# Kernel optimization log

Measured on AMD Instinct MI355X. Metric: run time of the kernel, lower is better.

## Reference

```python
import jax, jax.numpy as jnp
import numpy as np
import math

B, N, D, K = 4, 255, 256, 128
NODE_FEATURES_OFFSET = 128
MAX_Z = 101
NUM_EDGES = 2 * NODE_FEATURES_OFFSET + 1  # 257
NUM_DIR_KERNEL = 128  # FourierDirectionalEmbed num_kernel
ECFG_F = 20  # synthetic electron-config feature dim


def setup_inputs() -> dict:
    key = jax.random.key(0)
    ks = jax.random.split(key, 16)
    positions = jax.random.normal(ks[0], (B, N, 3), dtype=jnp.float32) * 3.0
    atomic_numbers = jax.random.randint(ks[1], (B, N), 1, MAX_Z, dtype=jnp.int32)
    s = 0.02
    emb_z = jax.random.normal(ks[2], (MAX_Z + 1, D), dtype=jnp.float32) * s
    electron_config = jax.random.uniform(ks[3], (MAX_Z + 1, ECFG_F), dtype=jnp.float32)
    config_W = jax.random.normal(ks[4], (ECFG_F, D), dtype=jnp.float32) * s
    config_b = jnp.zeros((D,), dtype=jnp.float32)
    mult_W = jax.random.normal(ks[5], (NODE_FEATURES_OFFSET, D), dtype=jnp.float32) * s
    charge_W = jax.random.normal(ks[6], (NODE_FEATURES_OFFSET, D), dtype=jnp.float32) * s
    gbf_means = jax.random.uniform(ks[7], (K,), dtype=jnp.float32, minval=0.0, maxval=7.0)
    gbf_stds = jax.random.uniform(ks[8], (K,), dtype=jnp.float32, minval=0.0, maxval=3.0)
    gbf_mul = jax.random.normal(ks[9], (NUM_EDGES,), dtype=jnp.float32).at[0].set(0.0)  # padding_idx=0
    gbf_bias = (jax.random.normal(ks[10], (NUM_EDGES,), dtype=jnp.float32) * 0.1).at[0].set(0.0)
    proj1_W = jax.random.normal(ks[11], (K, K), dtype=jnp.float32) * (1.0 / math.sqrt(K))
    proj1_b = jnp.zeros((K,), dtype=jnp.float32)
    proj2_W = jax.random.normal(ks[12], (K, D), dtype=jnp.float32) * (1.0 / math.sqrt(K))
    proj2_b = jnp.zeros((D,), dtype=jnp.float32)
    dir_W = jax.random.normal(ks[13], (2 * NUM_DIR_KERNEL, D), dtype=jnp.float32) * (1.0 / math.sqrt(2 * NUM_DIR_KERNEL))
    dir_b = jnp.zeros((D,), dtype=jnp.float32)
    return dict(positions=positions, atomic_numbers=atomic_numbers, emb_z=emb_z,
                electron_config=electron_config, config_W=config_W, config_b=config_b,
                mult_W=mult_W, charge_W=charge_W, gbf_means=gbf_means, gbf_stds=gbf_stds,
                gbf_mul=gbf_mul, gbf_bias=gbf_bias, proj1_W=proj1_W, proj1_b=proj1_b,
                proj2_W=proj2_W, proj2_b=proj2_b, dir_W=dir_W, dir_b=dir_b)


def _angular_freqs():
    min_angle = 1e-4
    half = NUM_DIR_KERNEL // 2
    wl_az = jnp.exp(jnp.linspace(math.log(2 * min_angle), math.log(2 * 2 * math.pi), half))
    wl_po = jnp.exp(jnp.linspace(math.log(2 * min_angle), math.log(2 * math.pi), half))
    return (2 * math.pi / wl_az).astype(jnp.float32), (2 * math.pi / wl_po).astype(jnp.float32)


def _forward(positions, atomic_numbers, emb_z, electron_config, config_W, config_b,
             mult_W, charge_W, gbf_means, gbf_stds, gbf_mul, gbf_bias,
             proj1_W, proj1_b, proj2_W, proj2_b, dir_W, dir_b):
    b = positions.shape[0]
    # add graph-level (CLS) token: zero position, z = MAX_Z = 101
    pos = jnp.concatenate([jnp.zeros_like(positions[:, :1]), positions], axis=1)  # [B,Np,3]
    z = jnp.concatenate([jnp.full_like(atomic_numbers[:, :1], MAX_Z), atomic_numbers], axis=1)  # [B,Np]
    npad = pos.shape[1]

    # --- node embedding: nuclear + electronic + multiplicity(1) + charge(0) ---
    elec = electron_config[z] @ config_W + config_b            # [B,Np,D]
    elec = elec.at[:, 0, :].set(0.0)                            # cls_token row zeroed
    node = emb_z[z] + elec + mult_W[1] + charge_W[0]           # [B,Np,D]

    # --- pairwise geometry: directions[b,i,j] = pos[j] - pos[i] ---
    d = pos[:, None, :, :] - pos[:, :, None, :]                # [B,Np,Np,3]
    sq = jnp.sum(d * d, axis=-1)
    dist = jnp.sqrt(sq + 1e-12)                                # [B,Np,Np]
    nd = d / (dist[..., None] + 1e-5)                          # normed directions, eps per source
    eye = jnp.eye(npad, dtype=bool)[None, :, :]
    x_safe = jnp.where(eye, 1.0, nd[..., 0])
    y_safe = jnp.where(eye, 0.0, nd[..., 1])
    azimuth = jnp.arctan2(y_safe, x_safe)                      # [B,Np,Np]
    polar = jnp.arccos(jnp.clip(nd[..., 2], -1.0 + 1e-6, 1.0 - 1e-6))

    # --- FourierDirectionalEmbed ---
    f_az, f_po = _angular_freqs()
    ph_az = azimuth[..., None] * f_az                          # [B,Np,Np,64]
    ph_po = polar[..., None] * f_po
    sinusoids = jnp.concatenate([jnp.sin(ph_az), jnp.cos(ph_az),
                                 jnp.sin(ph_po), jnp.cos(ph_po)], axis=-1)  # [B,Np,Np,256]
    dir_out = sinusoids @ dir_W + dir_b                        # [B,Np,Np,D]

    # --- Gaussian3DEmbed ---
    zi = z[:, :, None]
    zj = z[:, None, :] + NODE_FEATURES_OFFSET
    mul = gbf_mul[zi] + gbf_mul[zj]                            # sum over the 2 edge-type entries
    bias = gbf_bias[zi] + gbf_bias[zj]                         # [B,Np,Np]
    gx = (mul * dist + bias)[..., None]                        # [B,Np,Np,1] -> broadcast to K
    std = jnp.abs(gbf_stds) + 0.01
    pi_c = 3.14159
    gauss = jnp.exp(-0.5 * ((gx - gbf_means) / std) ** 2) / ((2 * pi_c) ** 0.5 * std)  # [B,Np,Np,K]
    h = jax.nn.gelu(gauss @ proj1_W + proj1_b, approximate=False)
    gbf_out = h @ proj2_W + proj2_b                            # [B,Np,Np,D]

    return node, gbf_out, dir_out


def reference(positions, atomic_numbers, emb_z, electron_config, config_W, config_b,
              mult_W, charge_W, gbf_means, gbf_stds, gbf_mul, gbf_bias,
              proj1_W, proj1_b, proj2_W, proj2_b, dir_W, dir_b):
    return _forward(positions, atomic_numbers, emb_z, electron_config, config_W, config_b,
                    mult_W, charge_W, gbf_means, gbf_stds, gbf_mul, gbf_bias,
                    proj1_W, proj1_b, proj2_W, proj2_b, dir_W, dir_b)
```

## Files before the change

kernel.cpp:

```cpp
#include <hip/hip_runtime.h>
#include <math.h>

typedef __bf16 bf16x8 __attribute__((ext_vector_type(8)));
typedef __bf16 bf16x4 __attribute__((ext_vector_type(4)));
typedef float f32x4 __attribute__((ext_vector_type(4)));

#define PI_D 3.14159265358979323846

__global__ void prep_kernel(const float* __restrict__ dir_W,
                            const float* __restrict__ proj1_W,
                            const float* __restrict__ proj2_W,
                            const float* __restrict__ gbf_stds,
                            __bf16* __restrict__ dirP, __bf16* __restrict__ p1P,
                            __bf16* __restrict__ p2P,
                            float* __restrict__ f_az, float* __restrict__ f_po,
                            float* __restrict__ inv_std, float* __restrict__ coef) {
  int tid = threadIdx.x + blockIdx.x * blockDim.x;
  int nth = gridDim.x * blockDim.x;
  for (int o = tid; o < 256 * 256; o += nth) {
    int j = o & 7, l = (o >> 3) & 63, ks = (o >> 9) & 7, nt = o >> 12;
    int d = nt * 16 + (l & 15);
    int s = ks * 32 + (l >> 4) * 8 + j;
    dirP[o] = (__bf16)dir_W[s * 256 + d];
  }
  for (int o = tid; o < 128 * 128; o += nth) {
    int j = o & 7, l = (o >> 3) & 63, ks = (o >> 9) & 3, nt = o >> 11;
    int ko = nt * 16 + (l & 15);
    int ki = ks * 32 + (l >> 4) * 8 + j;
    p1P[o] = (__bf16)proj1_W[ki * 128 + ko];
  }
  for (int o = tid; o < 128 * 256; o += nth) {
    int j = o & 7, l = (o >> 3) & 63, ks = (o >> 9) & 3, nt = o >> 11;
    int d = nt * 16 + (l & 15);
    int k = ks * 32 + (l >> 4) * 8 + j;
    p2P[o] = (__bf16)proj2_W[k * 256 + d];
  }
  if (blockIdx.x == 0 && threadIdx.x < 64) {
    int q = threadIdx.x;
    double l0 = log(2.0 * 1e-4);
    double l1a = log(2.0 * 2.0 * PI_D);
    double l1p = log(2.0 * PI_D);
    double ta = l0 + (l1a - l0) * (double)q / 63.0;
    double tp = l0 + (l1p - l0) * (double)q / 63.0;
    f_az[q] = (float)(2.0 * PI_D / exp(ta));
    f_po[q] = (float)(2.0 * PI_D / exp(tp));
  }
  if (blockIdx.x == 1 && threadIdx.x < 128) {
    int k = threadIdx.x;
    float sd = fabsf(gbf_stds[k]) + 0.01f;
    inv_std[k] = 1.0f / sd;
    coef[k] = (float)(1.0 / (sqrt(2.0 * 3.14159) * (double)sd));
  }
}

__global__ void node_kernel(const int* __restrict__ an, const float* __restrict__ emb_z,
                            const float* __restrict__ ec, const float* __restrict__ cW,
                            const float* __restrict__ cb, const float* __restrict__ mult_W,
                            const float* __restrict__ charge_W, float* __restrict__ out_node) {
  int bi = blockIdx.x;
  int b = bi >> 8, i = bi & 255;
  int d = threadIdx.x;
  int z = (i == 0) ? 101 : an[b * 255 + i - 1];
  float elec = 0.0f;
  if (i != 0) {
    for (int f = 0; f < 20; ++f) elec += ec[z * 20 + f] * cW[f * 256 + d];
    elec += cb[d];
  }
  float v = emb_z[z * 256 + d] + elec + mult_W[256 + d] + charge_W[d];
  out_node[(size_t)bi * 256 + d] = v;
}

__global__ __launch_bounds__(256, 4) void pair_kernel(
    const float* __restrict__ positions, const int* __restrict__ atomic_numbers,
    const float* __restrict__ gbf_means, const float* __restrict__ gbf_mul,
    const float* __restrict__ gbf_bias, const float* __restrict__ proj1_b,
    const float* __restrict__ proj2_b, const float* __restrict__ dir_b,
    const __bf16* __restrict__ dirP, const __bf16* __restrict__ p1P,
    const __bf16* __restrict__ p2P, const float* __restrict__ f_az,
    const float* __restrict__ f_po, const float* __restrict__ inv_stdv,
    const float* __restrict__ coefv, float* __restrict__ out_gbf,
    float* __restrict__ out_dir) {
  __shared__ __align__(16) __bf16 buf[64 * 136];
  __shared__ float s_az[64], s_po[64], s_gx[64];

  const int tid = threadIdx.x;
  const int bid = blockIdx.x;
  const int jt = bid & 3;
  const int i = (bid >> 2) & 255;
  const int b = bid >> 10;
  const int j0 = jt * 64;
  const long pairbase = ((long)(b * 256 + i)) * 256 + j0;

  const int lane = tid & 63, wv = tid >> 6;
  const int lr = lane & 15, kb = lane >> 4;

  if (tid < 64) {
    int p = tid, j = j0 + p;
    float pxi = 0.f, pyi = 0.f, pzi = 0.f, pxj = 0.f, pyj = 0.f, pzj = 0.f;
    if (i != 0) { const float* q = positions + ((size_t)b * 255 + (i - 1)) * 3; pxi = q[0]; pyi = q[1]; pzi = q[2]; }
    if (j != 0) { const float* q = positions + ((size_t)b * 255 + (j - 1)) * 3; pxj = q[0]; pyj = q[1]; pzj = q[2]; }
    float dx = pxj - pxi, dy = pyj - pyi, dz = pzj - pzi;
    float sq = dx * dx + dy * dy + dz * dz;
    float dist = sqrtf(sq + 1e-12f);
    float inv = 1.0f / (dist + 1e-5f);
    float ndx = dx * inv, ndy = dy * inv, ndz = dz * inv;
    bool diag = (i == j);
    float xs = diag ? 1.0f : ndx;
    float ys = diag ? 0.0f : ndy;
    s_az[p] = atan2f(ys, xs);
    float cz = fminf(fmaxf(ndz, -1.0f + 1e-6f), 1.0f - 1e-6f);
    s_po[p] = acosf(cz);
    int zi = (i == 0) ? 101 : atomic_numbers[b * 255 + i - 1];
    int zj = ((j == 0) ? 101 : atomic_numbers[b * 255 + j - 1]) + 128;
    float mul = gbf_mul[zi] + gbf_mul[zj];
    float bia = gbf_bias[zi] + gbf_bias[zj];
    s_gx[p] = mul * dist + bia;
  }
  __syncthreads();

  f32x4 acc[4][4];
#pragma unroll
  for (int mtl = 0; mtl < 4; ++mtl)
#pragma unroll
    for (int np = 0; np < 4; ++np) acc[mtl][np] = (f32x4){0.f, 0.f, 0.f, 0.f};

  for (int half = 0; half < 2; ++half) {
#pragma unroll
    for (int it = 0; it < 2; ++it) {
      int job = tid + it * 256;
      int p = job >> 3, g = job & 7;
      int q0 = g * 8;
      float ang = half ? s_po[p] : s_az[p];
      const float* ft = half ? f_po : f_az;
      bf16x8 sv, cv;
#pragma unroll
      for (int t = 0; t < 8; ++t) {
        float ph = ang * ft[q0 + t];
        double r = (double)ph * 0.15915494309189535;
        double fr = r - rint(r);
        float frf = (float)fr;
        sv[t] = (__bf16)__builtin_amdgcn_sinf(frf);
        cv[t] = (__bf16)__builtin_amdgcn_cosf(frf);
      }
      *(bf16x8*)(buf + p * 136 + q0) = sv;
      *(bf16x8*)(buf + p * 136 + 64 + q0) = cv;
    }
    __syncthreads();
#pragma unroll
    for (int ksl = 0; ksl < 4; ++ksl) {
      int ks = half * 4 + ksl;
      bf16x8 bfr[4];
#pragma unroll
      for (int np = 0; np < 4; ++np)
        bfr[np] = *(const bf16x8*)(buf + (np * 16 + lr) * 136 + ksl * 32 + kb * 8);
#pragma unroll
      for (int mtl = 0; mtl < 4; ++mtl) {
        int mtile = mtl * 4 + wv;
        bf16x8 af = *(const bf16x8*)(dirP + (((size_t)mtile * 8 + ks) * 64 + lane) * 8);
#pragma unroll
        for (int np = 0; np < 4; ++np)
          acc[mtl][np] = __builtin_amdgcn_mfma_f32_16x16x32_bf16(af, bfr[np], acc[mtl][np], 0, 0, 0);
      }
    }
    __syncthreads();
  }

#pragma unroll
  for (int mtl = 0; mtl < 4; ++mtl) {
    int dcol0 = (mtl * 4 + wv) * 16 + kb * 4;
    f32x4 bias = *(const f32x4*)(dir_b + dcol0);
#pragma unroll
    for (int np = 0; np < 4; ++np) {
      f32x4 v = acc[mtl][np] + bias;
      *(f32x4*)(out_dir + (pairbase + np * 16 + lr) * 256 + dcol0) = v;
    }
  }

#pragma unroll
  for (int it = 0; it < 4; ++it) {
    int job = tid + it * 256;
    int p = job >> 4, g = job & 15;
    int k0 = g * 8;
    float gx = s_gx[p];
    bf16x8 gv;
#pragma unroll
    for (int t = 0; t < 8; ++t) {
      int k = k0 + t;
      float x = (gx - gbf_means[k]) * inv_stdv[k];
      gv[t] = (__bf16)(exp2f(-0.72134752044448170f * x * x) * coefv[k]);
    }
    *(bf16x8*)(buf + p * 136 + k0) = gv;
  }
  __syncthreads();

  f32x4 acc1[2][4];
#pragma unroll
  for (int mtl = 0; mtl < 2; ++mtl)
#pragma unroll
    for (int np = 0; np < 4; ++np) acc1[mtl][np] = (f32x4){0.f, 0.f, 0.f, 0.f};
#pragma unroll
  for (int ksl = 0; ksl < 4; ++ksl) {
    bf16x8 bfr[4];
#pragma unroll
    for (int np = 0; np < 4; ++np)
      bfr[np] = *(const bf16x8*)(buf + (np * 16 + lr) * 136 + ksl * 32 + kb * 8);
#pragma unroll
    for (int mtl = 0; mtl < 2; ++mtl) {
      int mtile = mtl * 4 + wv;
      bf16x8 af = *(const bf16x8*)(p1P + (((size_t)mtile * 4 + ksl) * 64 + lane) * 8);
#pragma unroll
      for (int np = 0; np < 4; ++np)
        acc1[mtl][np] = __builtin_amdgcn_mfma_f32_16x16x32_bf16(af, bfr[np], acc1[mtl][np], 0, 0, 0);
    }
  }
  __syncthreads();

#pragma unroll
  for (int mtl = 0; mtl < 2; ++mtl) {
    int ko0 = (mtl * 4 + wv) * 16 + kb * 4;
    f32x4 pb = *(const f32x4*)(proj1_b + ko0);
#pragma unroll
    for (int np = 0; np < 4; ++np) {
      f32x4 hv = acc1[mtl][np] + pb;
      bf16x4 hb;
#pragma unroll
      for (int r = 0; r < 4; ++r) {
        float v = hv[r];
        v = 0.5f * v * (1.0f + erff(v * 0.70710678118654752f));
        hb[r] = (__bf16)v;
      }
      *(bf16x4*)(buf + (np * 16 + lr) * 136 + ko0) = hb;
    }
  }
  __syncthreads();

  f32x4 acc2[4][4];
#pragma unroll
  for (int mtl = 0; mtl < 4; ++mtl)
#pragma unroll
    for (int np = 0; np < 4; ++np) acc2[mtl][np] = (f32x4){0.f, 0.f, 0.f, 0.f};
#pragma unroll
  for (int ksl = 0; ksl < 4; ++ksl) {
    bf16x8 bfr[4];
#pragma unroll
    for (int np = 0; np < 4; ++np)
      bfr[np] = *(const bf16x8*)(buf + (np * 16 + lr) * 136 + ksl * 32 + kb * 8);
#pragma unroll
    for (int mtl = 0; mtl < 4; ++mtl) {
      int mtile = mtl * 4 + wv;
      bf16x8 af = *(const bf16x8*)(p2P + (((size_t)mtile * 4 + ksl) * 64 + lane) * 8);
#pragma unroll
      for (int np = 0; np < 4; ++np)
        acc2[mtl][np] = __builtin_amdgcn_mfma_f32_16x16x32_bf16(af, bfr[np], acc2[mtl][np], 0, 0, 0);
    }
  }
#pragma unroll
  for (int mtl = 0; mtl < 4; ++mtl) {
    int dcol0 = (mtl * 4 + wv) * 16 + kb * 4;
    f32x4 bias = *(const f32x4*)(proj2_b + dcol0);
#pragma unroll
    for (int np = 0; np < 4; ++np) {
      f32x4 v = acc2[mtl][np] + bias;
      *(f32x4*)(out_gbf + (pairbase + np * 16 + lr) * 256 + dcol0) = v;
    }
  }
}

extern "C" void kernel_launch(void* const* d_in, const int* in_sizes, int n_in,
                              void* d_out, int out_size, void* d_ws, size_t ws_size,
                              hipStream_t stream) {
  const float* positions = (const float*)d_in[0];
  const int* atomic_numbers = (const int*)d_in[1];
  const float* emb_z = (const float*)d_in[2];
  const float* electron_config = (const float*)d_in[3];
  const float* config_W = (const float*)d_in[4];
  const float* config_b = (const float*)d_in[5];
  const float* mult_W = (const float*)d_in[6];
  const float* charge_W = (const float*)d_in[7];
  const float* gbf_means = (const float*)d_in[8];
  const float* gbf_stds = (const float*)d_in[9];
  const float* gbf_mul = (const float*)d_in[10];
  const float* gbf_bias = (const float*)d_in[11];
  const float* proj1_W = (const float*)d_in[12];
  const float* proj1_b = (const float*)d_in[13];
  const float* proj2_W = (const float*)d_in[14];
  const float* proj2_b = (const float*)d_in[15];
  const float* dir_W = (const float*)d_in[16];
  const float* dir_b = (const float*)d_in[17];

  float* out = (float*)d_out;
  float* out_node = out;
  float* out_gbf = out + 262144;
  float* out_dir = out + 262144 + 67108864;

  char* ws = (char*)d_ws;
  __bf16* dirP = (__bf16*)(ws);
  __bf16* p1P = (__bf16*)(ws + 131072);
  __bf16* p2P = (__bf16*)(ws + 131072 + 32768);
  float* f_az = (float*)(ws + 229376);
  float* f_po = (float*)(ws + 229376 + 256);
  float* inv_std = (float*)(ws + 229376 + 512);
  float* coef = (float*)(ws + 229376 + 1024);

  prep_kernel<<<64, 256, 0, stream>>>(dir_W, proj1_W, proj2_W, gbf_stds, dirP, p1P,
                                      p2P, f_az, f_po, inv_std, coef);
  node_kernel<<<1024, 256, 0, stream>>>(atomic_numbers, emb_z, electron_config,
                                        config_W, config_b, mult_W, charge_W, out_node);
  pair_kernel<<<4096, 256, 0, stream>>>(positions, atomic_numbers, gbf_means, gbf_mul,
                                        gbf_bias, proj1_b, proj2_b, dir_b, dirP, p1P,
                                        p2P, f_az, f_po, inv_std, coef, out_gbf, out_dir);
}
```

Measured before the change: 166.9 us.

## Split fused pair kernel into separate directional and Gaussian kernels

```diff
diff --git a/kernel.cpp b/kernel.cpp
--- a/kernel.cpp
+++ b/kernel.cpp
@@ -70,18 +70,12 @@
   out_node[(size_t)bi * 256 + d] = v;
 }
 
-__global__ __launch_bounds__(256, 4) void pair_kernel(
-    const float* __restrict__ positions, const int* __restrict__ atomic_numbers,
-    const float* __restrict__ gbf_means, const float* __restrict__ gbf_mul,
-    const float* __restrict__ gbf_bias, const float* __restrict__ proj1_b,
-    const float* __restrict__ proj2_b, const float* __restrict__ dir_b,
-    const __bf16* __restrict__ dirP, const __bf16* __restrict__ p1P,
-    const __bf16* __restrict__ p2P, const float* __restrict__ f_az,
-    const float* __restrict__ f_po, const float* __restrict__ inv_stdv,
-    const float* __restrict__ coefv, float* __restrict__ out_gbf,
-    float* __restrict__ out_dir) {
-  __shared__ __align__(16) __bf16 buf[64 * 136];
-  __shared__ float s_az[64], s_po[64], s_gx[64];
+__global__ __launch_bounds__(256, 4) void dir_kernel(
+    const float* __restrict__ positions, const float* __restrict__ dir_b,
+    const __bf16* __restrict__ dirP, const float* __restrict__ f_az,
+    const float* __restrict__ f_po, float* __restrict__ out_dir) {
+  __shared__ __align__(16) __bf16 sin_t[64 * 264];
+  __shared__ float s_az[64], s_po[64];
 
   const int tid = threadIdx.x;
   const int bid = blockIdx.x;
@@ -90,7 +84,6 @@
   const int b = bid >> 10;
   const int j0 = jt * 64;
   const long pairbase = ((long)(b * 256 + i)) * 256 + j0;
-
   const int lane = tid & 63, wv = tid >> 6;
   const int lr = lane & 15, kb = lane >> 4;
 
@@ -110,6 +103,93 @@
     s_az[p] = atan2f(ys, xs);
     float cz = fminf(fmaxf(ndz, -1.0f + 1e-6f), 1.0f - 1e-6f);
     s_po[p] = acosf(cz);
+  }
+  __syncthreads();
+
+  for (int it = 0; it < 4; ++it) {
+    int job = tid + it * 256;
+    int p = job >> 4, g = job & 15;
+    bool az = g < 8;
+    int q0 = (g & 7) * 8;
+    float ang = az ? s_az[p] : s_po[p];
+    const float* ft = az ? f_az : f_po;
+    bf16x8 sv, cv;
+#pragma unroll
+    for (int t = 0; t < 8; ++t) {
+      float ph = ang * ft[q0 + t];
+      double r = (double)ph * 0.15915494309189535;
+      double fr = r - rint(r);
+      float frf = (float)fr;
+      sv[t] = (__bf16)__builtin_amdgcn_sinf(frf);
+      cv[t] = (__bf16)__builtin_amdgcn_cosf(frf);
+    }
+    int base = p * 264 + (az ? 0 : 128) + q0;
+    *(bf16x8*)(sin_t + base) = sv;
+    *(bf16x8*)(sin_t + base + 64) = cv;
+  }
+  __syncthreads();
+
+  f32x4 acc[4][4];
+#pragma unroll
+  for (int mtl = 0; mtl < 4; ++mtl)
+#pragma unroll
+    for (int np = 0; np < 4; ++np) acc[mtl][np] = (f32x4){0.f, 0.f, 0.f, 0.f};
+#pragma unroll
+  for (int ks = 0; ks < 8; ++ks) {
+    bf16x8 bfr[4];
+#pragma unroll
+    for (int np = 0; np < 4; ++np)
+      bfr[np] = *(const bf16x8*)(sin_t + (np * 16 + lr) * 264 + ks * 32 + kb * 8);
+#pragma unroll
+    for (int mtl = 0; mtl < 4; ++mtl) {
+      int mtile = mtl * 4 + wv;
+      bf16x8 af = *(const bf16x8*)(dirP + (((size_t)mtile * 8 + ks) * 64 + lane) * 8);
+#pragma unroll
+      for (int np = 0; np < 4; ++np)
+        acc[mtl][np] = __builtin_amdgcn_mfma_f32_16x16x32_bf16(af, bfr[np], acc[mtl][np], 0, 0, 0);
+    }
+  }
+#pragma unroll
+  for (int mtl = 0; mtl < 4; ++mtl) {
+    int dcol0 = (mtl * 4 + wv) * 16 + kb * 4;
+    f32x4 bias = *(const f32x4*)(dir_b + dcol0);
+#pragma unroll
+    for (int np = 0; np < 4; ++np) {
+      f32x4 v = acc[mtl][np] + bias;
+      *(f32x4*)(out_dir + (pairbase + np * 16 + lr) * 256 + dcol0) = v;
+    }
+  }
+}
+
+__global__ __launch_bounds__(256, 4) void gbf_kernel(
+    const float* __restrict__ positions, const int* __restrict__ atomic_numbers,
+    const float* __restrict__ gbf_means, const float* __restrict__ gbf_mul,
+    const float* __restrict__ gbf_bias, const float* __restrict__ proj1_b,
+    const float* __restrict__ proj2_b, const __bf16* __restrict__ p1P,
+    const __bf16* __restrict__ p2P, const float* __restrict__ inv_stdv,
+    const float* __restrict__ coefv, float* __restrict__ out_gbf) {
+  __shared__ __align__(16) __bf16 g_t[64 * 136];
+  __shared__ __align__(16) __bf16 h_t[64 * 136];
+  __shared__ float s_gx[64];
+
+  const int tid = threadIdx.x;
+  const int bid = blockIdx.x;
+  const int jt = bid & 3;
+  const int i = (bid >> 2) & 255;
+  const int b = bid >> 10;
+  const int j0 = jt * 64;
+  const long pairbase = ((long)(b * 256 + i)) * 256 + j0;
+  const int lane = tid & 63, wv = tid >> 6;
+  const int lr = lane & 15, kb = lane >> 4;
+
+  if (tid < 64) {
+    int p = tid, j = j0 + p;
+    float pxi = 0.f, pyi = 0.f, pzi = 0.f, pxj = 0.f, pyj = 0.f, pzj = 0.f;
+    if (i != 0) { const float* q = positions + ((size_t)b * 255 + (i - 1)) * 3; pxi = q[0]; pyi = q[1]; pzi = q[2]; }
+    if (j != 0) { const float* q = positions + ((size_t)b * 255 + (j - 1)) * 3; pxj = q[0]; pyj = q[1]; pzj = q[2]; }
+    float dx = pxj - pxi, dy = pyj - pyi, dz = pzj - pzi;
+    float sq = dx * dx + dy * dy + dz * dz;
+    float dist = sqrtf(sq + 1e-12f);
     int zi = (i == 0) ? 101 : atomic_numbers[b * 255 + i - 1];
     int zj = ((j == 0) ? 101 : atomic_numbers[b * 255 + j - 1]) + 128;
     float mul = gbf_mul[zi] + gbf_mul[zj];
@@ -117,64 +197,6 @@
     s_gx[p] = mul * dist + bia;
   }
   __syncthreads();
-
-  f32x4 acc[4][4];
-#pragma unroll
-  for (int mtl = 0; mtl < 4; ++mtl)
-#pragma unroll
-    for (int np = 0; np < 4; ++np) acc[mtl][np] = (f32x4){0.f, 0.f, 0.f, 0.f};
-
-  for (int half = 0; half < 2; ++half) {
-#pragma unroll
-    for (int it = 0; it < 2; ++it) {
-      int job = tid + it * 256;
-      int p = job >> 3, g = job & 7;
-      int q0 = g * 8;
-      float ang = half ? s_po[p] : s_az[p];
-      const float* ft = half ? f_po : f_az;
-      bf16x8 sv, cv;
-#pragma unroll
-      for (int t = 0; t < 8; ++t) {
-        float ph = ang * ft[q0 + t];
-        double r = (double)ph * 0.15915494309189535;
-        double fr = r - rint(r);
-        float frf = (float)fr;
-        sv[t] = (__bf16)__builtin_amdgcn_sinf(frf);
-        cv[t] = (__bf16)__builtin_amdgcn_cosf(frf);
-      }
-      *(bf16x8*)(buf + p * 136 + q0) = sv;
-      *(bf16x8*)(buf + p * 136 + 64 + q0) = cv;
-    }
-    __syncthreads();
-#pragma unroll
-    for (int ksl = 0; ksl < 4; ++ksl) {
-      int ks = half * 4 + ksl;
-      bf16x8 bfr[4];
-#pragma unroll
-      for (int np = 0; np < 4; ++np)
-        bfr[np] = *(const bf16x8*)(buf + (np * 16 + lr) * 136 + ksl * 32 + kb * 8);
-#pragma unroll
-      for (int mtl = 0; mtl < 4; ++mtl) {
-        int mtile = mtl * 4 + wv;
-        bf16x8 af = *(const bf16x8*)(dirP + (((size_t)mtile * 8 + ks) * 64 + lane) * 8);
-#pragma unroll
-        for (int np = 0; np < 4; ++np)
-          acc[mtl][np] = __builtin_amdgcn_mfma_f32_16x16x32_bf16(af, bfr[np], acc[mtl][np], 0, 0, 0);
-      }
-    }
-    __syncthreads();
-  }
-
-#pragma unroll
-  for (int mtl = 0; mtl < 4; ++mtl) {
-    int dcol0 = (mtl * 4 + wv) * 16 + kb * 4;
-    f32x4 bias = *(const f32x4*)(dir_b + dcol0);
-#pragma unroll
-    for (int np = 0; np < 4; ++np) {
-      f32x4 v = acc[mtl][np] + bias;
-      *(f32x4*)(out_dir + (pairbase + np * 16 + lr) * 256 + dcol0) = v;
-    }
-  }
 
 #pragma unroll
   for (int it = 0; it < 4; ++it) {
@@ -189,7 +211,7 @@
       float x = (gx - gbf_means[k]) * inv_stdv[k];
       gv[t] = (__bf16)(exp2f(-0.72134752044448170f * x * x) * coefv[k]);
     }
-    *(bf16x8*)(buf + p * 136 + k0) = gv;
+    *(bf16x8*)(g_t + p * 136 + k0) = gv;
   }
   __syncthreads();
 
@@ -203,7 +225,7 @@
     bf16x8 bfr[4];
 #pragma unroll
     for (int np = 0; np < 4; ++np)
-      bfr[np] = *(const bf16x8*)(buf + (np * 16 + lr) * 136 + ksl * 32 + kb * 8);
+      bfr[np] = *(const bf16x8*)(g_t + (np * 16 + lr) * 136 + ksl * 32 + kb * 8);
 #pragma unroll
     for (int mtl = 0; mtl < 2; ++mtl) {
       int mtile = mtl * 4 + wv;
@@ -213,7 +235,6 @@
         acc1[mtl][np] = __builtin_amdgcn_mfma_f32_16x16x32_bf16(af, bfr[np], acc1[mtl][np], 0, 0, 0);
     }
   }
-  __syncthreads();
 
 #pragma unroll
   for (int mtl = 0; mtl < 2; ++mtl) {
@@ -229,7 +250,7 @@
         v = 0.5f * v * (1.0f + erff(v * 0.70710678118654752f));
         hb[r] = (__bf16)v;
       }
-      *(bf16x4*)(buf + (np * 16 + lr) * 136 + ko0) = hb;
+      *(bf16x4*)(h_t + (np * 16 + lr) * 136 + ko0) = hb;
     }
   }
   __syncthreads();
@@ -244,7 +265,7 @@
     bf16x8 bfr[4];
 #pragma unroll
     for (int np = 0; np < 4; ++np)
-      bfr[np] = *(const bf16x8*)(buf + (np * 16 + lr) * 136 + ksl * 32 + kb * 8);
+      bfr[np] = *(const bf16x8*)(h_t + (np * 16 + lr) * 136 + ksl * 32 + kb * 8);
 #pragma unroll
     for (int mtl = 0; mtl < 4; ++mtl) {
       int mtile = mtl * 4 + wv;
@@ -304,9 +325,10 @@
 
   prep_kernel<<<64, 256, 0, stream>>>(dir_W, proj1_W, proj2_W, gbf_stds, dirP, p1P,
                                       p2P, f_az, f_po, inv_std, coef);
+  dir_kernel<<<4096, 256, 0, stream>>>(positions, dir_b, dirP, f_az, f_po, out_dir);
+  gbf_kernel<<<4096, 256, 0, stream>>>(positions, atomic_numbers, gbf_means, gbf_mul,
+                                       gbf_bias, proj1_b, proj2_b, p1P, p2P, inv_std,
+                                       coef, out_gbf);
   node_kernel<<<1024, 256, 0, stream>>>(atomic_numbers, emb_z, electron_config,
                                         config_W, config_b, mult_W, charge_W, out_node);
-  pair_kernel<<<4096, 256, 0, stream>>>(positions, atomic_numbers, gbf_means, gbf_mul,
-                                        gbf_bias, proj1_b, proj2_b, dir_b, dirP, p1P,
-                                        p2P, f_az, f_po, inv_std, coef, out_gbf, out_dir);
-}
+}
```

Result: slower. 176.6 us (+5.8%).
